# Kernel tuning notes

Measured on AMD Instinct MI355X. Metric: run time of the kernel, lower is better.

Reference implementation:

```python
import jax, jax.numpy as jnp
import numpy as np

N, IN_DIM, OUT_DIM, HEADS = 3072, 512, 64, 8
EDGE_PROB = 0.01
NEG_SLOPE = 0.2


def setup_inputs() -> dict:
    key = jax.random.key(0)
    k1, k2, k3, k4, k5 = jax.random.split(key, 5)
    x = jax.random.normal(k1, (N, IN_DIM), dtype=jnp.float32)
    # sparse-ish dense adjacency mask with self-loops
    adj = (jax.random.uniform(k2, (N, N)) < EDGE_PROB).astype(jnp.float32)
    adj = jnp.maximum(adj, jnp.eye(N, dtype=jnp.float32))
    W = jax.random.normal(k3, (HEADS, IN_DIM, OUT_DIM), dtype=jnp.float32) * 0.1
    a_src = jax.random.normal(k4, (HEADS, OUT_DIM), dtype=jnp.float32) * 0.1
    a_dst = jax.random.normal(k5, (HEADS, OUT_DIM), dtype=jnp.float32) * 0.1
    return {"x": x, "adj": adj, "W": W, "a_src": a_src, "a_dst": a_dst}


def reference(x, adj, W, a_src, a_dst):
    # per-head linear projection: [H, N, OUT]
    h = jnp.einsum("ni,hio->hno", x, W)
    # attention logits e_ij = LeakyReLU(a_src . h_i + a_dst . h_j)
    f_src = jnp.einsum("hno,ho->hn", h, a_src)  # [H, N]
    f_dst = jnp.einsum("hno,ho->hn", h, a_dst)  # [H, N]
    e = f_src[:, :, None] + f_dst[:, None, :]   # [H, N, N]
    e = jax.nn.leaky_relu(e, negative_slope=NEG_SLOPE)
    # mask non-edges, row-softmax over neighbors
    e = jnp.where(adj[None] > 0, e, jnp.float32(-1e9))
    att = jax.nn.softmax(e, axis=-1)             # [H, N, N]
    # aggregate neighbor features per head
    out = jnp.einsum("hij,hjo->hio", att, h)     # [H, N, OUT]
    # concat heads along feature dim -> [N, H*OUT]
    return out.transpose(1, 0, 2).reshape(N, HEADS * OUT_DIM)
```

## Files before the change

### kernel.cpp

```cpp
#include <hip/hip_runtime.h>

#define N_NODES 3072
#define IN_DIM 512
#define OUT_DIM 64
#define HEADS 8
#define NEG_SLOPE 0.2f
#define MAX_E 128

typedef __attribute__((ext_vector_type(8))) short bf16x8;
typedef __attribute__((ext_vector_type(4))) float f32x4;

#define XFRAG_TILES (N_NODES / 16)
#define KTILES (IN_DIM / 32)
#define XFRAG_THREADS (XFRAG_TILES * KTILES * 64)
#define WFRAG_THREADS (HEADS * KTILES * 4 * 64)

__device__ inline unsigned short f2bf(float f) {
    union { float f; unsigned u; } v; v.f = f;
    unsigned r = (v.u + 0x7FFF + ((v.u >> 16) & 1)) >> 16;
    return (unsigned short)r;
}

__global__ __launch_bounds__(256) void gat_prep(
    const float* __restrict__ x, const float* __restrict__ W,
    short* __restrict__ xfrag, short* __restrict__ wfrag) {
    int tid = blockIdx.x * 256 + threadIdx.x;
    if (tid < XFRAG_THREADS) {
        int lane = tid & 63;
        int kt = (tid >> 6) & (KTILES - 1);
        int rt = tid >> 10;
        int m = rt * 16 + (lane & 15);
        int k0 = kt * 32 + (lane >> 4) * 8;
        const float4* xp = (const float4*)(x + (size_t)m * IN_DIM + k0);
        float4 v0 = xp[0], v1 = xp[1];
        bf16x8 r;
        r[0] = (short)f2bf(v0.x); r[1] = (short)f2bf(v0.y);
        r[2] = (short)f2bf(v0.z); r[3] = (short)f2bf(v0.w);
        r[4] = (short)f2bf(v1.x); r[5] = (short)f2bf(v1.y);
        r[6] = (short)f2bf(v1.z); r[7] = (short)f2bf(v1.w);
        ((bf16x8*)xfrag)[tid] = r;
    } else {
        int t2 = tid - XFRAG_THREADS;
        if (t2 >= WFRAG_THREADS) return;
        int lane = t2 & 63;
        int c = (t2 >> 6) & 3;
        int kt = (t2 >> 8) & (KTILES - 1);
        int head = t2 >> 12;
        int n = c * 16 + (lane & 15);
        int k0 = kt * 32 + (lane >> 4) * 8;
        const float* wp = W + ((size_t)head * IN_DIM + k0) * OUT_DIM + n;
        bf16x8 r;
#pragma unroll
        for (int j = 0; j < 8; ++j) r[j] = (short)f2bf(wp[(size_t)j * OUT_DIM]);
        ((bf16x8*)wfrag)[t2] = r;
    }
}

__global__ __launch_bounds__(256) void gat_proj(
    const short* __restrict__ xfrag, const short* __restrict__ wfrag,
    const float* __restrict__ a_src, const float* __restrict__ a_dst,
    unsigned short* __restrict__ hb, float* __restrict__ fsrc, float* __restrict__ fdst) {
    __shared__ float hs[32][OUT_DIM + 1];

    const int t = threadIdx.x;
    const int lane = t & 63;
    const int w = t >> 6;
    const int head = blockIdx.y;
    const int m0 = blockIdx.x * 32;
    const int rt0 = blockIdx.x * 2;

    const bf16x8* xa = (const bf16x8*)xfrag + (size_t)rt0 * 16 * 64 + lane;
    const bf16x8* wb = (const bf16x8*)wfrag + ((size_t)head * KTILES * 4 + w) * 64 + lane;

    f32x4 acc0 = {0.f, 0.f, 0.f, 0.f};
    f32x4 acc1 = {0.f, 0.f, 0.f, 0.f};
#pragma unroll
    for (int kt = 0; kt < KTILES; ++kt) {
        bf16x8 a0 = xa[kt * 64];
        bf16x8 a1 = xa[(16 + kt) * 64];
        bf16x8 b  = wb[kt * 4 * 64];
        acc0 = __builtin_amdgcn_mfma_f32_16x16x32_bf16(a0, b, acc0, 0, 0, 0);
        acc1 = __builtin_amdgcn_mfma_f32_16x16x32_bf16(a1, b, acc1, 0, 0, 0);
    }

    const int col = w * 16 + (lane & 15);
    const int r0 = (lane >> 4) * 4;
    unsigned short* hp = hb + (size_t)m0 * (HEADS * OUT_DIM) + head * OUT_DIM + col;
#pragma unroll
    for (int i2 = 0; i2 < 4; ++i2) {
        hs[r0 + i2][col] = acc0[i2];
        hs[r0 + 16 + i2][col] = acc1[i2];
        hp[(size_t)(r0 + i2) * (HEADS * OUT_DIM)] = f2bf(acc0[i2]);
        hp[(size_t)(r0 + 16 + i2) * (HEADS * OUT_DIM)] = f2bf(acc1[i2]);
    }
    __syncthreads();

    {
        const float* av = (t < 128 ? a_src : a_dst) + head * OUT_DIM;
        const int tt = t & 127;
        const int row = tt >> 2, part = tt & 3;
        float s = 0.f;
#pragma unroll
        for (int n = 0; n < 16; ++n) s += hs[row][part * 16 + n] * av[part * 16 + n];
        s += __shfl_xor(s, 1, 64);
        s += __shfl_xor(s, 2, 64);
        if (part == 0) {
            float* dst = (t < 128 ? fsrc : fdst);
            dst[head * N_NODES + m0 + row] = s;
        }
    }
}

__global__ __launch_bounds__(256) void gat_agg(
    const float* __restrict__ adj, const unsigned short* __restrict__ hb,
    const float* __restrict__ fsrc, const float* __restrict__ fdst,
    float* __restrict__ out) {
    __shared__ int s_idx[MAX_E];
    __shared__ float s_p[HEADS][MAX_E];
    __shared__ int s_cnt;

    const int i = blockIdx.x;
    const int t = threadIdx.x;
    if (t == 0) s_cnt = 0;
    __syncthreads();

    const float4* arow4 = (const float4*)(adj + (size_t)i * N_NODES);
#pragma unroll
    for (int it = 0; it < 3; ++it) {
        const int jj = t + it * 256;
        float4 v = arow4[jj];
        const int j = jj * 4;
        if (v.x > 0.f) { int s = atomicAdd(&s_cnt, 1); if (s < MAX_E) s_idx[s] = j; }
        if (v.y > 0.f) { int s = atomicAdd(&s_cnt, 1); if (s < MAX_E) s_idx[s] = j + 1; }
        if (v.z > 0.f) { int s = atomicAdd(&s_cnt, 1); if (s < MAX_E) s_idx[s] = j + 2; }
        if (v.w > 0.f) { int s = atomicAdd(&s_cnt, 1); if (s < MAX_E) s_idx[s] = j + 3; }
    }
    __syncthreads();
    const int E = min(s_cnt, MAX_E);

    const int w = t >> 6;
    const int lane = t & 63;
    const int half = lane >> 5;
    const int sl = lane & 31;
    const int head = 2 * w + half;

    const float fi = fsrc[head * N_NODES + i];

    float m = -1e30f;
    for (int k = sl; k < E; k += 32) {
        float e = fi + fdst[head * N_NODES + s_idx[k]];
        e = e > 0.f ? e : NEG_SLOPE * e;
        s_p[head][k] = e;
        m = fmaxf(m, e);
    }
#pragma unroll
    for (int o = 16; o; o >>= 1) m = fmaxf(m, __shfl_xor(m, o, 64));

    float sum = 0.f;
    for (int k = sl; k < E; k += 32) {
        float p = __expf(s_p[head][k] - m);
        s_p[head][k] = p;
        sum += p;
    }
#pragma unroll
    for (int o = 16; o; o >>= 1) sum += __shfl_xor(sum, o, 64);
    const float inv = 1.f / sum;

    __syncthreads();

    const unsigned short* hbase = hb + head * OUT_DIM + sl * 2;
    float a0 = 0.f, a1 = 0.f;
#pragma unroll 8
    for (int k = 0; k < E; ++k) {
        const int j = s_idx[k];
        const float p = s_p[head][k];
        const unsigned u = *(const unsigned*)(hbase + (size_t)j * (HEADS * OUT_DIM));
        a0 = fmaf(p, __uint_as_float(u << 16), a0);
        a1 = fmaf(p, __uint_as_float(u & 0xffff0000u), a1);
    }
    float2 r = {a0 * inv, a1 * inv};
    *(float2*)(out + (size_t)i * (HEADS * OUT_DIM) + head * OUT_DIM + sl * 2) = r;
}

extern "C" void kernel_launch(void* const* d_in, const int* in_sizes, int n_in,
                              void* d_out, int out_size, void* d_ws, size_t ws_size,
                              hipStream_t stream) {
    const float* x     = (const float*)d_in[0];
    const float* adj   = (const float*)d_in[1];
    const float* W     = (const float*)d_in[2];
    const float* a_src = (const float*)d_in[3];
    const float* a_dst = (const float*)d_in[4];
    float* out = (float*)d_out;

    float* fsrc = (float*)d_ws;
    float* fdst = fsrc + HEADS * N_NODES;
    unsigned short* hb = (unsigned short*)(fdst + HEADS * N_NODES);
    short* xfrag = (short*)(hb + (size_t)N_NODES * HEADS * OUT_DIM);
    short* wfrag = xfrag + (size_t)XFRAG_TILES * KTILES * 64 * 8;

    gat_prep<<<(XFRAG_THREADS + WFRAG_THREADS) / 256, 256, 0, stream>>>(
        x, W, xfrag, wfrag);
    gat_proj<<<dim3(N_NODES / 32, HEADS), 256, 0, stream>>>(
        xfrag, wfrag, a_src, a_dst, hb, fsrc, fdst);
    gat_agg<<<N_NODES, 256, 0, stream>>>(adj, hb, fsrc, fdst, out);
}
```

Baseline: 108.2 us.

## Fuse prep, projection and aggregation into one cooperative persistent kernel

The three separate launches (bf16 fragment prep, MFMA projection, neighbour aggregation) are merged into a single cooperative kernel with 768 blocks, separated by grid-wide syncs. The aggregation phase becomes a grid-stride loop over nodes. This targets launch overhead and the tail gaps between kernels. In exchange it adds the cost of grid barriers and caps occupancy at a fixed block count, which could underfill the device during the aggregation phase.

Measured after the change: 370.6 us. 3.42x slower.

```diff
diff --git a/kernel.cpp b/kernel.cpp
--- a/kernel.cpp
+++ b/kernel.cpp
@@ -1,4 +1,7 @@
 #include <hip/hip_runtime.h>
+#include <hip/hip_cooperative_groups.h>
+
+namespace cg = cooperative_groups;
 
 #define N_NODES 3072
 #define IN_DIM 512
@@ -6,6 +9,7 @@
 #define HEADS 8
 #define NEG_SLOPE 0.2f
 #define MAX_E 128
+#define NBLK 768
 
 typedef __attribute__((ext_vector_type(8))) short bf16x8;
 typedef __attribute__((ext_vector_type(4))) float f32x4;
@@ -21,87 +25,95 @@
     return (unsigned short)r;
 }
 
-__global__ __launch_bounds__(256) void gat_prep(
-    const float* __restrict__ x, const float* __restrict__ W,
-    short* __restrict__ xfrag, short* __restrict__ wfrag) {
-    int tid = blockIdx.x * 256 + threadIdx.x;
-    if (tid < XFRAG_THREADS) {
-        int lane = tid & 63;
-        int kt = (tid >> 6) & (KTILES - 1);
-        int rt = tid >> 10;
-        int m = rt * 16 + (lane & 15);
-        int k0 = kt * 32 + (lane >> 4) * 8;
-        const float4* xp = (const float4*)(x + (size_t)m * IN_DIM + k0);
-        float4 v0 = xp[0], v1 = xp[1];
-        bf16x8 r;
-        r[0] = (short)f2bf(v0.x); r[1] = (short)f2bf(v0.y);
-        r[2] = (short)f2bf(v0.z); r[3] = (short)f2bf(v0.w);
-        r[4] = (short)f2bf(v1.x); r[5] = (short)f2bf(v1.y);
-        r[6] = (short)f2bf(v1.z); r[7] = (short)f2bf(v1.w);
-        ((bf16x8*)xfrag)[tid] = r;
-    } else {
-        int t2 = tid - XFRAG_THREADS;
-        if (t2 >= WFRAG_THREADS) return;
-        int lane = t2 & 63;
-        int c = (t2 >> 6) & 3;
-        int kt = (t2 >> 8) & (KTILES - 1);
-        int head = t2 >> 12;
-        int n = c * 16 + (lane & 15);
-        int k0 = kt * 32 + (lane >> 4) * 8;
-        const float* wp = W + ((size_t)head * IN_DIM + k0) * OUT_DIM + n;
-        bf16x8 r;
-#pragma unroll
-        for (int j = 0; j < 8; ++j) r[j] = (short)f2bf(wp[(size_t)j * OUT_DIM]);
-        ((bf16x8*)wfrag)[t2] = r;
-    }
-}
-
-__global__ __launch_bounds__(256) void gat_proj(
-    const short* __restrict__ xfrag, const short* __restrict__ wfrag,
-    const float* __restrict__ a_src, const float* __restrict__ a_dst,
-    unsigned short* __restrict__ hb, float* __restrict__ fsrc, float* __restrict__ fdst) {
+__global__ __launch_bounds__(256, 3) void gat_fused(
+    const float* __restrict__ x, const float* __restrict__ adj,
+    const float* __restrict__ W, const float* __restrict__ a_src,
+    const float* __restrict__ a_dst,
+    short* __restrict__ xfrag, short* __restrict__ wfrag,
+    unsigned short* __restrict__ hb, float* __restrict__ fsrc,
+    float* __restrict__ fdst, float* __restrict__ out) {
     __shared__ float hs[32][OUT_DIM + 1];
+    __shared__ int s_idx[MAX_E];
+    __shared__ float s_p[HEADS][MAX_E];
+    __shared__ int s_cnt;
 
     const int t = threadIdx.x;
+    const int b = blockIdx.x;
     const int lane = t & 63;
     const int w = t >> 6;
-    const int head = blockIdx.y;
-    const int m0 = blockIdx.x * 32;
-    const int rt0 = blockIdx.x * 2;
-
-    const bf16x8* xa = (const bf16x8*)xfrag + (size_t)rt0 * 16 * 64 + lane;
-    const bf16x8* wb = (const bf16x8*)wfrag + ((size_t)head * KTILES * 4 + w) * 64 + lane;
-
-    f32x4 acc0 = {0.f, 0.f, 0.f, 0.f};
-    f32x4 acc1 = {0.f, 0.f, 0.f, 0.f};
-#pragma unroll
-    for (int kt = 0; kt < KTILES; ++kt) {
-        bf16x8 a0 = xa[kt * 64];
-        bf16x8 a1 = xa[(16 + kt) * 64];
-        bf16x8 b  = wb[kt * 4 * 64];
-        acc0 = __builtin_amdgcn_mfma_f32_16x16x32_bf16(a0, b, acc0, 0, 0, 0);
-        acc1 = __builtin_amdgcn_mfma_f32_16x16x32_bf16(a1, b, acc1, 0, 0, 0);
+
+    {
+        const int tid = b * 256 + t;
+        {
+            const int l = tid & 63;
+            const int kt = (tid >> 6) & (KTILES - 1);
+            const int rt = tid >> 10;
+            const int m = rt * 16 + (l & 15);
+            const int k0 = kt * 32 + (l >> 4) * 8;
+            const float4* xp = (const float4*)(x + (size_t)m * IN_DIM + k0);
+            float4 v0 = xp[0], v1 = xp[1];
+            bf16x8 r;
+            r[0] = (short)f2bf(v0.x); r[1] = (short)f2bf(v0.y);
+            r[2] = (short)f2bf(v0.z); r[3] = (short)f2bf(v0.w);
+            r[4] = (short)f2bf(v1.x); r[5] = (short)f2bf(v1.y);
+            r[6] = (short)f2bf(v1.z); r[7] = (short)f2bf(v1.w);
+            ((bf16x8*)xfrag)[tid] = r;
+        }
+        if (tid < WFRAG_THREADS) {
+            const int l = tid & 63;
+            const int c = (tid >> 6) & 3;
+            const int kt = (tid >> 8) & (KTILES - 1);
+            const int head = tid >> 12;
+            const int n = c * 16 + (l & 15);
+            const int k0 = kt * 32 + (l >> 4) * 8;
+            const float* wp = W + ((size_t)head * IN_DIM + k0) * OUT_DIM + n;
+            bf16x8 r;
+#pragma unroll
+            for (int j = 0; j < 8; ++j) r[j] = (short)f2bf(wp[(size_t)j * OUT_DIM]);
+            ((bf16x8*)wfrag)[tid] = r;
+        }
     }
-
-    const int col = w * 16 + (lane & 15);
-    const int r0 = (lane >> 4) * 4;
-    unsigned short* hp = hb + (size_t)m0 * (HEADS * OUT_DIM) + head * OUT_DIM + col;
-#pragma unroll
-    for (int i2 = 0; i2 < 4; ++i2) {
-        hs[r0 + i2][col] = acc0[i2];
-        hs[r0 + 16 + i2][col] = acc1[i2];
-        hp[(size_t)(r0 + i2) * (HEADS * OUT_DIM)] = f2bf(acc0[i2]);
-        hp[(size_t)(r0 + 16 + i2) * (HEADS * OUT_DIM)] = f2bf(acc1[i2]);
-    }
-    __syncthreads();
+    __threadfence();
+    cg::this_grid().sync();
 
     {
+        const int head = b / 96;
+        const int rtp = b % 96;
+        const int m0 = rtp * 32;
+        const int rt0 = rtp * 2;
+
+        const bf16x8* xa = (const bf16x8*)xfrag + (size_t)rt0 * 16 * 64 + lane;
+        const bf16x8* wb = (const bf16x8*)wfrag + ((size_t)head * KTILES * 4 + w) * 64 + lane;
+
+        f32x4 acc0 = {0.f, 0.f, 0.f, 0.f};
+        f32x4 acc1 = {0.f, 0.f, 0.f, 0.f};
+#pragma unroll 4
+        for (int kt = 0; kt < KTILES; ++kt) {
+            bf16x8 a0 = xa[kt * 64];
+            bf16x8 a1 = xa[(16 + kt) * 64];
+            bf16x8 bv = wb[kt * 4 * 64];
+            acc0 = __builtin_amdgcn_mfma_f32_16x16x32_bf16(a0, bv, acc0, 0, 0, 0);
+            acc1 = __builtin_amdgcn_mfma_f32_16x16x32_bf16(a1, bv, acc1, 0, 0, 0);
+        }
+
+        const int col = w * 16 + (lane & 15);
+        const int r0 = (lane >> 4) * 4;
+        unsigned short* hp = hb + (size_t)m0 * (HEADS * OUT_DIM) + head * OUT_DIM + col;
+#pragma unroll
+        for (int i2 = 0; i2 < 4; ++i2) {
+            hs[r0 + i2][col] = acc0[i2];
+            hs[r0 + 16 + i2][col] = acc1[i2];
+            hp[(size_t)(r0 + i2) * (HEADS * OUT_DIM)] = f2bf(acc0[i2]);
+            hp[(size_t)(r0 + 16 + i2) * (HEADS * OUT_DIM)] = f2bf(acc1[i2]);
+        }
+        __syncthreads();
+
         const float* av = (t < 128 ? a_src : a_dst) + head * OUT_DIM;
         const int tt = t & 127;
         const int row = tt >> 2, part = tt & 3;
         float s = 0.f;
 #pragma unroll
-        for (int n = 0; n < 16; ++n) s += hs[row][part * 16 + n] * av[part * 16 + n];
+        for (int n2 = 0; n2 < 16; ++n2) s += hs[row][part * 16 + n2] * av[part * 16 + n2];
         s += __shfl_xor(s, 1, 64);
         s += __shfl_xor(s, 2, 64);
         if (part == 0) {
@@ -109,77 +121,68 @@
             dst[head * N_NODES + m0 + row] = s;
         }
     }
-}
-
-__global__ __launch_bounds__(256) void gat_agg(
-    const float* __restrict__ adj, const unsigned short* __restrict__ hb,
-    const float* __restrict__ fsrc, const float* __restrict__ fdst,
-    float* __restrict__ out) {
-    __shared__ int s_idx[MAX_E];
-    __shared__ float s_p[HEADS][MAX_E];
-    __shared__ int s_cnt;
-
-    const int i = blockIdx.x;
-    const int t = threadIdx.x;
-    if (t == 0) s_cnt = 0;
-    __syncthreads();
-
-    const float4* arow4 = (const float4*)(adj + (size_t)i * N_NODES);
-#pragma unroll
-    for (int it = 0; it < 3; ++it) {
-        const int jj = t + it * 256;
-        float4 v = arow4[jj];
-        const int j = jj * 4;
-        if (v.x > 0.f) { int s = atomicAdd(&s_cnt, 1); if (s < MAX_E) s_idx[s] = j; }
-        if (v.y > 0.f) { int s = atomicAdd(&s_cnt, 1); if (s < MAX_E) s_idx[s] = j + 1; }
-        if (v.z > 0.f) { int s = atomicAdd(&s_cnt, 1); if (s < MAX_E) s_idx[s] = j + 2; }
-        if (v.w > 0.f) { int s = atomicAdd(&s_cnt, 1); if (s < MAX_E) s_idx[s] = j + 3; }
+    __threadfence();
+    cg::this_grid().sync();
+
+    for (int i = b; i < N_NODES; i += NBLK) {
+        if (t == 0) s_cnt = 0;
+        __syncthreads();
+
+        const float4* arow4 = (const float4*)(adj + (size_t)i * N_NODES);
+#pragma unroll
+        for (int it = 0; it < 3; ++it) {
+            const int jj = t + it * 256;
+            float4 v = arow4[jj];
+            const int j = jj * 4;
+            if (v.x > 0.f) { int s = atomicAdd(&s_cnt, 1); if (s < MAX_E) s_idx[s] = j; }
+            if (v.y > 0.f) { int s = atomicAdd(&s_cnt, 1); if (s < MAX_E) s_idx[s] = j + 1; }
+            if (v.z > 0.f) { int s = atomicAdd(&s_cnt, 1); if (s < MAX_E) s_idx[s] = j + 2; }
+            if (v.w > 0.f) { int s = atomicAdd(&s_cnt, 1); if (s < MAX_E) s_idx[s] = j + 3; }
+        }
+        __syncthreads();
+        const int E = min(s_cnt, MAX_E);
+
+        const int half = lane >> 5;
+        const int sl = lane & 31;
+        const int head = 2 * w + half;
+
+        const float fi = fsrc[head * N_NODES + i];
+
+        float m = -1e30f;
+        for (int k = sl; k < E; k += 32) {
+            float e = fi + fdst[head * N_NODES + s_idx[k]];
+            e = e > 0.f ? e : NEG_SLOPE * e;
+            s_p[head][k] = e;
+            m = fmaxf(m, e);
+        }
+#pragma unroll
+        for (int o = 16; o; o >>= 1) m = fmaxf(m, __shfl_xor(m, o, 64));
+
+        float sum = 0.f;
+        for (int k = sl; k < E; k += 32) {
+            float p = __expf(s_p[head][k] - m);
+            s_p[head][k] = p;
+            sum += p;
+        }
+#pragma unroll
+        for (int o = 16; o; o >>= 1) sum += __shfl_xor(sum, o, 64);
+        const float inv = 1.f / sum;
+
+        __syncthreads();
+
+        const unsigned short* hbase = hb + head * OUT_DIM + sl * 2;
+        float a0 = 0.f, a1 = 0.f;
+#pragma unroll 8
+        for (int k = 0; k < E; ++k) {
+            const int j = s_idx[k];
+            const float p = s_p[head][k];
+            const unsigned u = *(const unsigned*)(hbase + (size_t)j * (HEADS * OUT_DIM));
+            a0 = fmaf(p, __uint_as_float(u << 16), a0);
+            a1 = fmaf(p, __uint_as_float(u & 0xffff0000u), a1);
+        }
+        float2 r2 = {a0 * inv, a1 * inv};
+        *(float2*)(out + (size_t)i * (HEADS * OUT_DIM) + head * OUT_DIM + sl * 2) = r2;
     }
-    __syncthreads();
-    const int E = min(s_cnt, MAX_E);
-
-    const int w = t >> 6;
-    const int lane = t & 63;
-    const int half = lane >> 5;
-    const int sl = lane & 31;
-    const int head = 2 * w + half;
-
-    const float fi = fsrc[head * N_NODES + i];
-
-    float m = -1e30f;
-    for (int k = sl; k < E; k += 32) {
-        float e = fi + fdst[head * N_NODES + s_idx[k]];
-        e = e > 0.f ? e : NEG_SLOPE * e;
-        s_p[head][k] = e;
-        m = fmaxf(m, e);
-    }
-#pragma unroll
-    for (int o = 16; o; o >>= 1) m = fmaxf(m, __shfl_xor(m, o, 64));
-
-    float sum = 0.f;
-    for (int k = sl; k < E; k += 32) {
-        float p = __expf(s_p[head][k] - m);
-        s_p[head][k] = p;
-        sum += p;
-    }
-#pragma unroll
-    for (int o = 16; o; o >>= 1) sum += __shfl_xor(sum, o, 64);
-    const float inv = 1.f / sum;
-
-    __syncthreads();
-
-    const unsigned short* hbase = hb + head * OUT_DIM + sl * 2;
-    float a0 = 0.f, a1 = 0.f;
-#pragma unroll 8
-    for (int k = 0; k < E; ++k) {
-        const int j = s_idx[k];
-        const float p = s_p[head][k];
-        const unsigned u = *(const unsigned*)(hbase + (size_t)j * (HEADS * OUT_DIM));
-        a0 = fmaf(p, __uint_as_float(u << 16), a0);
-        a1 = fmaf(p, __uint_as_float(u & 0xffff0000u), a1);
-    }
-    float2 r = {a0 * inv, a1 * inv};
-    *(float2*)(out + (size_t)i * (HEADS * OUT_DIM) + head * OUT_DIM + sl * 2) = r;
 }
 
 extern "C" void kernel_launch(void* const* d_in, const int* in_sizes, int n_in,
@@ -198,9 +201,9 @@
     short* xfrag = (short*)(hb + (size_t)N_NODES * HEADS * OUT_DIM);
     short* wfrag = xfrag + (size_t)XFRAG_TILES * KTILES * 64 * 8;
 
-    gat_prep<<<(XFRAG_THREADS + WFRAG_THREADS) / 256, 256, 0, stream>>>(
-        x, W, xfrag, wfrag);
-    gat_proj<<<dim3(N_NODES / 32, HEADS), 256, 0, stream>>>(
-        xfrag, wfrag, a_src, a_dst, hb, fsrc, fdst);
-    gat_agg<<<N_NODES, 256, 0, stream>>>(adj, hb, fsrc, fdst, out);
+    void* args[] = {(void*)&x, (void*)&adj, (void*)&W, (void*)&a_src, (void*)&a_dst,
+                    (void*)&xfrag, (void*)&wfrag, (void*)&hb, (void*)&fsrc,
+                    (void*)&fdst, (void*)&out};
+    hipLaunchCooperativeKernel((const void*)gat_fused, dim3(NBLK), dim3(256),
+                               args, 0, stream);
 }
```

## Fuse bf16 fragment prep into projection kernel, converting x and W on the fly

Applied to the files above, without the earlier changes.

Removes the separate prep kernel that converted x and W into MFMA-ordered bf16 fragments in workspace. The projection kernel now reads fp32 x and W directly, converts them to bf16 in registers and keeps all 16 W k-tiles in registers. This saves one launch and a workspace write/read round trip. In exchange, each of the 8 head blocks re-reads and re-converts the same fp32 x rows, W is read with strided scalar loads, and register pressure rises (launch bounds now request 3 blocks per CU).

New measurement: 144.4 us. +33.4%, slower.

```diff
diff --git a/kernel.cpp b/kernel.cpp
--- a/kernel.cpp
+++ b/kernel.cpp
@@ -6,14 +6,10 @@
 #define HEADS 8
 #define NEG_SLOPE 0.2f
 #define MAX_E 128
+#define KTILES (IN_DIM / 32)
 
 typedef __attribute__((ext_vector_type(8))) short bf16x8;
 typedef __attribute__((ext_vector_type(4))) float f32x4;
-
-#define XFRAG_TILES (N_NODES / 16)
-#define KTILES (IN_DIM / 32)
-#define XFRAG_THREADS (XFRAG_TILES * KTILES * 64)
-#define WFRAG_THREADS (HEADS * KTILES * 4 * 64)
 
 __device__ inline unsigned short f2bf(float f) {
     union { float f; unsigned u; } v; v.f = f;
@@ -21,45 +17,11 @@
     return (unsigned short)r;
 }
 
-__global__ __launch_bounds__(256) void gat_prep(
+__global__ __launch_bounds__(256, 3) void gat_proj(
     const float* __restrict__ x, const float* __restrict__ W,
-    short* __restrict__ xfrag, short* __restrict__ wfrag) {
-    int tid = blockIdx.x * 256 + threadIdx.x;
-    if (tid < XFRAG_THREADS) {
-        int lane = tid & 63;
-        int kt = (tid >> 6) & (KTILES - 1);
-        int rt = tid >> 10;
-        int m = rt * 16 + (lane & 15);
-        int k0 = kt * 32 + (lane >> 4) * 8;
-        const float4* xp = (const float4*)(x + (size_t)m * IN_DIM + k0);
-        float4 v0 = xp[0], v1 = xp[1];
-        bf16x8 r;
-        r[0] = (short)f2bf(v0.x); r[1] = (short)f2bf(v0.y);
-        r[2] = (short)f2bf(v0.z); r[3] = (short)f2bf(v0.w);
-        r[4] = (short)f2bf(v1.x); r[5] = (short)f2bf(v1.y);
-        r[6] = (short)f2bf(v1.z); r[7] = (short)f2bf(v1.w);
-        ((bf16x8*)xfrag)[tid] = r;
-    } else {
-        int t2 = tid - XFRAG_THREADS;
-        if (t2 >= WFRAG_THREADS) return;
-        int lane = t2 & 63;
-        int c = (t2 >> 6) & 3;
-        int kt = (t2 >> 8) & (KTILES - 1);
-        int head = t2 >> 12;
-        int n = c * 16 + (lane & 15);
-        int k0 = kt * 32 + (lane >> 4) * 8;
-        const float* wp = W + ((size_t)head * IN_DIM + k0) * OUT_DIM + n;
-        bf16x8 r;
-#pragma unroll
-        for (int j = 0; j < 8; ++j) r[j] = (short)f2bf(wp[(size_t)j * OUT_DIM]);
-        ((bf16x8*)wfrag)[t2] = r;
-    }
-}
-
-__global__ __launch_bounds__(256) void gat_proj(
-    const short* __restrict__ xfrag, const short* __restrict__ wfrag,
     const float* __restrict__ a_src, const float* __restrict__ a_dst,
-    unsigned short* __restrict__ hb, float* __restrict__ fsrc, float* __restrict__ fdst) {
+    unsigned short* __restrict__ hb, float* __restrict__ fsrc,
+    float* __restrict__ fdst) {
     __shared__ float hs[32][OUT_DIM + 1];
 
     const int t = threadIdx.x;
@@ -67,24 +29,49 @@
     const int w = t >> 6;
     const int head = blockIdx.y;
     const int m0 = blockIdx.x * 32;
-    const int rt0 = blockIdx.x * 2;
 
-    const bf16x8* xa = (const bf16x8*)xfrag + (size_t)rt0 * 16 * 64 + lane;
-    const bf16x8* wb = (const bf16x8*)wfrag + ((size_t)head * KTILES * 4 + w) * 64 + lane;
+    const int colr = lane & 15;
+    const int kq = lane >> 4;
+
+    bf16x8 wf[KTILES];
+    {
+        const float* wp0 = W + ((size_t)head * IN_DIM + kq * 8) * OUT_DIM + w * 16 + colr;
+#pragma unroll
+        for (int kt = 0; kt < KTILES; ++kt) {
+            const float* wp = wp0 + (size_t)kt * 32 * OUT_DIM;
+            bf16x8 r;
+#pragma unroll
+            for (int j = 0; j < 8; ++j) r[j] = (short)f2bf(wp[(size_t)j * OUT_DIM]);
+            wf[kt] = r;
+        }
+    }
+
+    const float* xr0 = x + (size_t)(m0 + colr) * IN_DIM + kq * 8;
+    const float* xr1 = xr0 + (size_t)16 * IN_DIM;
 
     f32x4 acc0 = {0.f, 0.f, 0.f, 0.f};
     f32x4 acc1 = {0.f, 0.f, 0.f, 0.f};
-#pragma unroll
+#pragma unroll 2
     for (int kt = 0; kt < KTILES; ++kt) {
-        bf16x8 a0 = xa[kt * 64];
-        bf16x8 a1 = xa[(16 + kt) * 64];
-        bf16x8 b  = wb[kt * 4 * 64];
-        acc0 = __builtin_amdgcn_mfma_f32_16x16x32_bf16(a0, b, acc0, 0, 0, 0);
-        acc1 = __builtin_amdgcn_mfma_f32_16x16x32_bf16(a1, b, acc1, 0, 0, 0);
+        const float4* p0 = (const float4*)(xr0 + kt * 32);
+        const float4* p1 = (const float4*)(xr1 + kt * 32);
+        float4 u0 = p0[0], u1 = p0[1];
+        float4 v0 = p1[0], v1 = p1[1];
+        bf16x8 a0, a1;
+        a0[0] = (short)f2bf(u0.x); a0[1] = (short)f2bf(u0.y);
+        a0[2] = (short)f2bf(u0.z); a0[3] = (short)f2bf(u0.w);
+        a0[4] = (short)f2bf(u1.x); a0[5] = (short)f2bf(u1.y);
+        a0[6] = (short)f2bf(u1.z); a0[7] = (short)f2bf(u1.w);
+        a1[0] = (short)f2bf(v0.x); a1[1] = (short)f2bf(v0.y);
+        a1[2] = (short)f2bf(v0.z); a1[3] = (short)f2bf(v0.w);
+        a1[4] = (short)f2bf(v1.x); a1[5] = (short)f2bf(v1.y);
+        a1[6] = (short)f2bf(v1.z); a1[7] = (short)f2bf(v1.w);
+        acc0 = __builtin_amdgcn_mfma_f32_16x16x32_bf16(a0, wf[kt], acc0, 0, 0, 0);
+        acc1 = __builtin_amdgcn_mfma_f32_16x16x32_bf16(a1, wf[kt], acc1, 0, 0, 0);
     }
 
-    const int col = w * 16 + (lane & 15);
-    const int r0 = (lane >> 4) * 4;
+    const int col = w * 16 + colr;
+    const int r0 = kq * 4;
     unsigned short* hp = hb + (size_t)m0 * (HEADS * OUT_DIM) + head * OUT_DIM + col;
 #pragma unroll
     for (int i2 = 0; i2 < 4; ++i2) {
@@ -195,12 +182,8 @@
     float* fsrc = (float*)d_ws;
     float* fdst = fsrc + HEADS * N_NODES;
     unsigned short* hb = (unsigned short*)(fdst + HEADS * N_NODES);
-    short* xfrag = (short*)(hb + (size_t)N_NODES * HEADS * OUT_DIM);
-    short* wfrag = xfrag + (size_t)XFRAG_TILES * KTILES * 64 * 8;
 
-    gat_prep<<<(XFRAG_THREADS + WFRAG_THREADS) / 256, 256, 0, stream>>>(
-        x, W, xfrag, wfrag);
     gat_proj<<<dim3(N_NODES / 32, HEADS), 256, 0, stream>>>(
-        xfrag, wfrag, a_src, a_dst, hb, fsrc, fdst);
+        x, W, a_src, a_dst, hb, fsrc, fdst);
     gat_agg<<<N_NODES, 256, 0, stream>>>(adj, hb, fsrc, fdst, out);
 }
```

## Move adjacency scan into projection kernel to overlap with MFMA projection

Applied to the files above, without the earlier changes.

The adjacency row scan that builds neighbor lists moves out of the aggregation kernel into extra blocks of the projection launch. The compacted indices and counts go to workspace, and the aggregation kernel only reads them. The aim is to overlap the memory-bound 37MB adjacency read with the compute-bound projection and shorten the aggregation kernel. In exchange it adds a global write and read of the index lists and some extra workspace.

After: 108.1 us. No clear change (-0.1%).

```diff
diff --git a/kernel.cpp b/kernel.cpp
--- a/kernel.cpp
+++ b/kernel.cpp
@@ -14,6 +14,7 @@
 #define KTILES (IN_DIM / 32)
 #define XFRAG_THREADS (XFRAG_TILES * KTILES * 64)
 #define WFRAG_THREADS (HEADS * KTILES * 4 * 64)
+#define PROJ_BLOCKS (N_NODES / 32 * HEADS)
 
 __device__ inline unsigned short f2bf(float f) {
     union { float f; unsigned u; } v; v.f = f;
@@ -56,46 +57,53 @@
     }
 }
 
-__global__ __launch_bounds__(256) void gat_proj(
+__global__ __launch_bounds__(256) void gat_proj_scan(
     const short* __restrict__ xfrag, const short* __restrict__ wfrag,
     const float* __restrict__ a_src, const float* __restrict__ a_dst,
-    unsigned short* __restrict__ hb, float* __restrict__ fsrc, float* __restrict__ fdst) {
+    const float* __restrict__ adj,
+    unsigned short* __restrict__ hb, float* __restrict__ fsrc,
+    float* __restrict__ fdst, int* __restrict__ e_idx, int* __restrict__ e_cnt) {
     __shared__ float hs[32][OUT_DIM + 1];
-
+    __shared__ int s_idx[MAX_E];
+    __shared__ int s_cnt;
+
+    const int b = blockIdx.x;
     const int t = threadIdx.x;
-    const int lane = t & 63;
-    const int w = t >> 6;
-    const int head = blockIdx.y;
-    const int m0 = blockIdx.x * 32;
-    const int rt0 = blockIdx.x * 2;
-
-    const bf16x8* xa = (const bf16x8*)xfrag + (size_t)rt0 * 16 * 64 + lane;
-    const bf16x8* wb = (const bf16x8*)wfrag + ((size_t)head * KTILES * 4 + w) * 64 + lane;
-
-    f32x4 acc0 = {0.f, 0.f, 0.f, 0.f};
-    f32x4 acc1 = {0.f, 0.f, 0.f, 0.f};
-#pragma unroll
-    for (int kt = 0; kt < KTILES; ++kt) {
-        bf16x8 a0 = xa[kt * 64];
-        bf16x8 a1 = xa[(16 + kt) * 64];
-        bf16x8 b  = wb[kt * 4 * 64];
-        acc0 = __builtin_amdgcn_mfma_f32_16x16x32_bf16(a0, b, acc0, 0, 0, 0);
-        acc1 = __builtin_amdgcn_mfma_f32_16x16x32_bf16(a1, b, acc1, 0, 0, 0);
-    }
-
-    const int col = w * 16 + (lane & 15);
-    const int r0 = (lane >> 4) * 4;
-    unsigned short* hp = hb + (size_t)m0 * (HEADS * OUT_DIM) + head * OUT_DIM + col;
-#pragma unroll
-    for (int i2 = 0; i2 < 4; ++i2) {
-        hs[r0 + i2][col] = acc0[i2];
-        hs[r0 + 16 + i2][col] = acc1[i2];
-        hp[(size_t)(r0 + i2) * (HEADS * OUT_DIM)] = f2bf(acc0[i2]);
-        hp[(size_t)(r0 + 16 + i2) * (HEADS * OUT_DIM)] = f2bf(acc1[i2]);
-    }
-    __syncthreads();
-
-    {
+
+    if (b < PROJ_BLOCKS) {
+        const int lane = t & 63;
+        const int w = t >> 6;
+        const int head = b / 96;
+        const int rtp = b % 96;
+        const int m0 = rtp * 32;
+        const int rt0 = rtp * 2;
+
+        const bf16x8* xa = (const bf16x8*)xfrag + (size_t)rt0 * 16 * 64 + lane;
+        const bf16x8* wb = (const bf16x8*)wfrag + ((size_t)head * KTILES * 4 + w) * 64 + lane;
+
+        f32x4 acc0 = {0.f, 0.f, 0.f, 0.f};
+        f32x4 acc1 = {0.f, 0.f, 0.f, 0.f};
+#pragma unroll
+        for (int kt = 0; kt < KTILES; ++kt) {
+            bf16x8 a0 = xa[kt * 64];
+            bf16x8 a1 = xa[(16 + kt) * 64];
+            bf16x8 bv = wb[kt * 4 * 64];
+            acc0 = __builtin_amdgcn_mfma_f32_16x16x32_bf16(a0, bv, acc0, 0, 0, 0);
+            acc1 = __builtin_amdgcn_mfma_f32_16x16x32_bf16(a1, bv, acc1, 0, 0, 0);
+        }
+
+        const int col = w * 16 + (lane & 15);
+        const int r0 = (lane >> 4) * 4;
+        unsigned short* hp = hb + (size_t)m0 * (HEADS * OUT_DIM) + head * OUT_DIM + col;
+#pragma unroll
+        for (int i2 = 0; i2 < 4; ++i2) {
+            hs[r0 + i2][col] = acc0[i2];
+            hs[r0 + 16 + i2][col] = acc1[i2];
+            hp[(size_t)(r0 + i2) * (HEADS * OUT_DIM)] = f2bf(acc0[i2]);
+            hp[(size_t)(r0 + 16 + i2) * (HEADS * OUT_DIM)] = f2bf(acc1[i2]);
+        }
+        __syncthreads();
+
         const float* av = (t < 128 ? a_src : a_dst) + head * OUT_DIM;
         const int tt = t & 127;
         const int row = tt >> 2, part = tt & 3;
@@ -108,35 +116,42 @@
             float* dst = (t < 128 ? fsrc : fdst);
             dst[head * N_NODES + m0 + row] = s;
         }
+    } else {
+        const int i = b - PROJ_BLOCKS;
+        if (t == 0) s_cnt = 0;
+        __syncthreads();
+
+        const float4* arow4 = (const float4*)(adj + (size_t)i * N_NODES);
+#pragma unroll
+        for (int it = 0; it < 3; ++it) {
+            const int jj = t + it * 256;
+            float4 v = arow4[jj];
+            const int j = jj * 4;
+            if (v.x > 0.f) { int s = atomicAdd(&s_cnt, 1); if (s < MAX_E) s_idx[s] = j; }
+            if (v.y > 0.f) { int s = atomicAdd(&s_cnt, 1); if (s < MAX_E) s_idx[s] = j + 1; }
+            if (v.z > 0.f) { int s = atomicAdd(&s_cnt, 1); if (s < MAX_E) s_idx[s] = j + 2; }
+            if (v.w > 0.f) { int s = atomicAdd(&s_cnt, 1); if (s < MAX_E) s_idx[s] = j + 3; }
+        }
+        __syncthreads();
+        const int E = min(s_cnt, MAX_E);
+        if (t < E) e_idx[(size_t)i * MAX_E + t] = s_idx[t];
+        if (t == 0) e_cnt[i] = E;
     }
 }
 
 __global__ __launch_bounds__(256) void gat_agg(
-    const float* __restrict__ adj, const unsigned short* __restrict__ hb,
+    const int* __restrict__ e_idx, const int* __restrict__ e_cnt,
+    const unsigned short* __restrict__ hb,
     const float* __restrict__ fsrc, const float* __restrict__ fdst,
     float* __restrict__ out) {
     __shared__ int s_idx[MAX_E];
     __shared__ float s_p[HEADS][MAX_E];
-    __shared__ int s_cnt;
 
     const int i = blockIdx.x;
     const int t = threadIdx.x;
-    if (t == 0) s_cnt = 0;
+    const int E = e_cnt[i];
+    if (t < E) s_idx[t] = e_idx[(size_t)i * MAX_E + t];
     __syncthreads();
-
-    const float4* arow4 = (const float4*)(adj + (size_t)i * N_NODES);
-#pragma unroll
-    for (int it = 0; it < 3; ++it) {
-        const int jj = t + it * 256;
-        float4 v = arow4[jj];
-        const int j = jj * 4;
-        if (v.x > 0.f) { int s = atomicAdd(&s_cnt, 1); if (s < MAX_E) s_idx[s] = j; }
-        if (v.y > 0.f) { int s = atomicAdd(&s_cnt, 1); if (s < MAX_E) s_idx[s] = j + 1; }
-        if (v.z > 0.f) { int s = atomicAdd(&s_cnt, 1); if (s < MAX_E) s_idx[s] = j + 2; }
-        if (v.w > 0.f) { int s = atomicAdd(&s_cnt, 1); if (s < MAX_E) s_idx[s] = j + 3; }
-    }
-    __syncthreads();
-    const int E = min(s_cnt, MAX_E);
 
     const int w = t >> 6;
     const int lane = t & 63;
@@ -197,10 +212,12 @@
     unsigned short* hb = (unsigned short*)(fdst + HEADS * N_NODES);
     short* xfrag = (short*)(hb + (size_t)N_NODES * HEADS * OUT_DIM);
     short* wfrag = xfrag + (size_t)XFRAG_TILES * KTILES * 64 * 8;
+    int* e_idx = (int*)(wfrag + (size_t)HEADS * KTILES * 4 * 64 * 8);
+    int* e_cnt = e_idx + (size_t)N_NODES * MAX_E;
 
     gat_prep<<<(XFRAG_THREADS + WFRAG_THREADS) / 256, 256, 0, stream>>>(
         x, W, xfrag, wfrag);
-    gat_proj<<<dim3(N_NODES / 32, HEADS), 256, 0, stream>>>(
-        xfrag, wfrag, a_src, a_dst, hb, fsrc, fdst);
-    gat_agg<<<N_NODES, 256, 0, stream>>>(adj, hb, fsrc, fdst, out);
-}
+    gat_proj_scan<<<PROJ_BLOCKS + N_NODES, 256, 0, stream>>>(
+        xfrag, wfrag, a_src, a_dst, adj, hb, fsrc, fdst, e_idx, e_cnt);
+    gat_agg<<<N_NODES, 256, 0, stream>>>(e_idx, e_cnt, hb, fsrc, fdst, out);
+}
```
